# Optimization experiments

Measured on AMD Instinct MI355X. Metric: run time of the kernel, lower is better.

The kernel has to match this reference:

```python
import jax, jax.numpy as jnp
import numpy as np


def setup_inputs() -> dict:
    key = jax.random.key(0)
    k1, k2, k3, k4 = jax.random.split(key, 4)
    B, N, Fin, Fout, K = 8, 256, 64, 64, 3
    H = jax.random.normal(k1, (B, N, N, Fin), dtype=jnp.float32)
    # static Chebyshev polynomial stacks T_0..T_{K-1} for origin / dest Laplacians
    cheb_L1 = jax.random.normal(k2, (K, N, N), dtype=jnp.float32) * 0.1
    cheb_L2 = jax.random.normal(k3, (K, N, N), dtype=jnp.float32) * 0.1
    # xavier_uniform over last two dims (fan_in=Fin, fan_out=Fout)
    limit = float(np.sqrt(6.0 / (Fin + Fout)))
    weights = jax.random.uniform(k4, (K, K, Fin, Fout), dtype=jnp.float32,
                                 minval=-limit, maxval=limit)
    bias = jnp.zeros((Fout,), dtype=jnp.float32)
    return {"H": H, "cheb_L1": cheb_L1, "cheb_L2": cheb_L2,
            "weights": weights, "bias": bias}


def reference(H, cheb_L1, cheb_L2, weights, bias):
    # H' = relu( sum_{i,j} T_i(L1) @_1 H @_2 T_j(L2) @_3 W_ij + b )
    # Step 1: left graph shift for all i at once: (K,B,N,N,F)
    H_x1 = jnp.einsum('kuv,bvwf->kbuwf', cheb_L1, H)
    # Step 2+3 fused: right shift by T_j, project by W_ij, accumulate over i,j
    out = jnp.einsum('kbuwf,lwz,klfo->buzo', H_x1, cheb_L2, weights)
    return jax.nn.relu(out + bias)
```

## Files before the change

kernel.cpp:

```cpp
#include <hip/hip_runtime.h>

typedef __attribute__((ext_vector_type(8))) short s16x8;
typedef __attribute__((ext_vector_type(4))) float f32x4;

#define MFMA16 __builtin_amdgcn_mfma_f32_16x16x32_bf16
#define WAITVM(N) asm volatile("s_waitcnt vmcnt(" #N ")" ::: "memory")
#define SBAR() asm volatile("s_barrier" ::: "memory")
#define WAITLGKM0() asm volatile("s_waitcnt lgkmcnt(0)" ::: "memory")
#define SCHEDB() __builtin_amdgcn_sched_barrier(0)

__device__ __forceinline__ short f2bf(float x) {
  union { float f; unsigned u; } c; c.f = x;
  unsigned r = (c.u + 0x7fffu + ((c.u >> 16) & 1u)) >> 16;
  return (short)r;
}

__device__ __forceinline__ void gld16(const void* g, void* l) {
  __builtin_amdgcn_global_load_lds(
      (const __attribute__((address_space(1))) unsigned*)g,
      (__attribute__((address_space(3))) unsigned*)l, 16, 0, 0);
}


__global__ __launch_bounds__(256) void k_cvt_l1(const float* __restrict__ L1,
                                                short* __restrict__ L1b) {
  int i = blockIdx.x * 256 + threadIdx.x;
  L1b[i] = f2bf(L1[i]);
}

__global__ __launch_bounds__(256) void k_build_l2cat(const float* __restrict__ L2,
                                                     short* __restrict__ L2cat) {
  __shared__ float t[32][33];
  const int l = blockIdx.z, w0 = blockIdx.x * 32, z0 = blockIdx.y * 32;
  const int tx = threadIdx.x, ty = threadIdx.y;
  const float* src = L2 + (size_t)l * 65536;
  for (int i = ty; i < 32; i += 8) t[i][tx] = src[(size_t)(w0 + i) * 256 + z0 + tx];
  __syncthreads();
  for (int i = ty; i < 32; i += 8)
    L2cat[(size_t)(z0 + i) * 768 + l * 256 + w0 + tx] = f2bf(t[tx][i]);
}

__global__ __launch_bounds__(256) void k_build_wt(const float* __restrict__ W,
                                                  short* __restrict__ WT) {
  for (int idx = threadIdx.x + blockIdx.x * 256; idx < 192 * 192; idx += 256 * gridDim.x) {
    int lo = idx / 192, kf = idx % 192;
    int l = lo / 64, o = lo & 63, k = kf / 64, f = kf & 63;
    WT[idx] = f2bf(W[(((size_t)(k * 3 + l) * 64 + f) << 6) + o]);
  }
}

__global__ __launch_bounds__(256) void k_cvt_ht(const float* __restrict__ H,
                                                short* __restrict__ HbT, int b0) {
  __shared__ float t[32][33];
  const int bc = blockIdx.z;
  const int wf0 = blockIdx.x * 32, v0 = blockIdx.y * 32;
  const int tx = threadIdx.x, ty = threadIdx.y;
  const float* src = H + ((size_t)(b0 + bc) * 256 + v0) * 16384;
  for (int i = ty; i < 32; i += 8) t[i][tx] = src[(size_t)i * 16384 + wf0 + tx];
  __syncthreads();
  short* dst = HbT + ((size_t)bc * 16384 + wf0) * 256;
  for (int i = ty; i < 32; i += 8) dst[(size_t)i * 256 + v0 + tx] = f2bf(t[tx][i]);
}

__global__ __launch_bounds__(256, 4) void k_s1(const short* __restrict__ L1b,
                                               const short* __restrict__ HbT,
                                               short* __restrict__ A2) {
  __shared__ __align__(16) short At[2][128 * 32];
  __shared__ __align__(16) short Bt[2][128 * 32];
  const int t = threadIdx.x, lane = t & 63, wid = t >> 6;
  const int n0 = blockIdx.x * 128;
  const int kk = blockIdx.y >> 1;
  const int u0 = (blockIdx.y & 1) * 128;
  const int bc = blockIdx.z;
  const short* Ag = L1b + (size_t)kk * 65536;
  const short* Bg = HbT + (size_t)bc * 16384 * 256;
  const int wm = wid >> 1, wn = wid & 1;
  const int srow = lane >> 2;
  const int selem = ((lane & 3) ^ ((lane >> 3) & 3)) * 8;
  const int koff = ((lane >> 4) ^ ((lane >> 1) & 3)) * 8;
  const int ar = lane & 15;
#pragma unroll
  for (int j = 0; j < 2; ++j) {
    const int rb = wid * 32 + j * 16;
    gld16(Ag + (size_t)(u0 + rb + srow) * 256 + selem, At[0] + rb * 32);
    gld16(Bg + (size_t)(n0 + rb + srow) * 256 + selem, Bt[0] + rb * 32);
  }
  __syncthreads();
  f32x4 acc[4][4] = {};
#pragma unroll
  for (int kt8 = 0; kt8 < 8; ++kt8) {
    const int cur = kt8 & 1;
    s16x8 a[4], b[4];
#pragma unroll
    for (int i = 0; i < 4; ++i)
      a[i] = *(const s16x8*)&At[cur][(wm * 64 + i * 16 + ar) * 32 + koff];
#pragma unroll
    for (int j = 0; j < 4; ++j)
      b[j] = *(const s16x8*)&Bt[cur][(wn * 64 + j * 16 + ar) * 32 + koff];
    if (kt8 < 7) {
#pragma unroll
      for (int j = 0; j < 2; ++j) {
        const int rb = wid * 32 + j * 16;
        gld16(Ag + (size_t)(u0 + rb + srow) * 256 + (kt8 + 1) * 32 + selem, At[cur ^ 1] + rb * 32);
        gld16(Bg + (size_t)(n0 + rb + srow) * 256 + (kt8 + 1) * 32 + selem, Bt[cur ^ 1] + rb * 32);
      }
    }
#pragma unroll
    for (int i = 0; i < 4; ++i)
#pragma unroll
      for (int j = 0; j < 4; ++j) acc[i][j] = MFMA16(a[i], b[j], acc[i][j], 0, 0, 0);
    __syncthreads();
  }
  const int cr = lane >> 4, cc = lane & 15;
#pragma unroll
  for (int i = 0; i < 4; ++i)
#pragma unroll
    for (int j = 0; j < 4; ++j) {
      const int ncol = n0 + wn * 64 + j * 16 + cc;
      const int w = ncol >> 6, f = ncol & 63;
#pragma unroll
      for (int r = 0; r < 4; ++r) {
        const int u = u0 + wm * 64 + i * 16 + cr * 4 + r;
        A2[(((size_t)bc * 256 + u) * 256 + w) * 192 + kk * 64 + f] = f2bf(acc[i][j][r]);
      }
    }
}

__global__ __launch_bounds__(512, 4) void k_s23(const short* __restrict__ A2,
                                                const short* __restrict__ WTg,
                                                const short* __restrict__ L2cat,
                                                const float* __restrict__ bias,
                                                float* __restrict__ out, int b0) {
  __shared__ __align__(16) short P[64 * 256];
  __shared__ __align__(16) short AtS[8][3][32 * 32];
  short* Ws = P;
  const int t = threadIdx.x, lane = t & 63, wid = t >> 6;
  const int bul = blockIdx.x;
  const int ar = lane & 15, cc = ar, cr = lane >> 4, sl = lane & 7, ks = lane >> 4;
  const int srow = lane >> 2;
  const int selem = ((lane & 3) ^ ((lane >> 3) & 3)) * 8;
  const int koff = ((lane >> 4) ^ ((lane >> 1) & 3)) * 8;
  const short* A2g = A2 + (size_t)bul * 49152;

#define P1S(tt, bi)                                                                        \
  do {                                                                                     \
    gld16(A2g + (size_t)(wid * 32 + srow) * 192 + (tt) * 32 + selem, &AtS[wid][bi][0]);    \
    gld16(A2g + (size_t)(wid * 32 + 16 + srow) * 192 + (tt) * 32 + selem,                  \
          &AtS[wid][bi][512]);                                                             \
  } while (0)
#define P2S(tt, bi)                                                                        \
  do {                                                                                     \
    gld16(L2cat + (size_t)(wid * 32 + srow) * 768 + (tt) * 32 + selem, &AtS[wid][bi][0]);  \
    gld16(L2cat + (size_t)(wid * 32 + 16 + srow) * 768 + (tt) * 32 + selem,                \
          &AtS[wid][bi][512]);                                                             \
  } while (0)

  f32x4 acc2[2][4] = {};
#pragma unroll
  for (int l = 0; l < 3; ++l) {
    const short* WTl = WTg + (size_t)l * 64 * 192;
    for (int s = wid; s < 24; s += 8) {
      const int t6 = s / 4, g = (s & 3) * 16;
      gld16(WTl + (size_t)(g + srow) * 192 + t6 * 32 + selem, Ws + ((size_t)t6 * 64 + g) * 32);
    }
    P1S(0, 0);
    P1S(1, 1);
    P1S(2, 2);
    WAITVM(6);
    SBAR();

    f32x4 acc[4][2] = {};
#pragma unroll
    for (int kt6 = 0; kt6 < 6; ++kt6) {
      if (kt6 < 4) { WAITVM(4); } else if (kt6 == 4) { WAITVM(2); } else { WAITVM(0); }
      const short* stc = &AtS[wid][kt6 % 3][0];
      s16x8 a0 = *(const s16x8*)&stc[(0 + ar) * 32 + koff];
      s16x8 a1 = *(const s16x8*)&stc[(16 + ar) * 32 + koff];
#pragma unroll
      for (int j2 = 0; j2 < 4; ++j2) {
        s16x8 b = *(const s16x8*)&Ws[((size_t)kt6 * 64 + j2 * 16 + ar) * 32 + koff];
        acc[j2][0] = MFMA16(a0, b, acc[j2][0], 0, 0, 0);
        acc[j2][1] = MFMA16(a1, b, acc[j2][1], 0, 0, 0);
      }
      SCHEDB();
      if (kt6 == 0) { P1S(3, 0); } else if (kt6 == 1) { P1S(4, 1); } else if (kt6 == 2) { P1S(5, 2); }
    }
    WAITLGKM0();
    SBAR();

    P2S(l * 8 + 0, 0);
    P2S(l * 8 + 1, 1);
    P2S(l * 8 + 2, 2);

#pragma unroll
    for (int j2 = 0; j2 < 4; ++j2)
#pragma unroll
      for (int i = 0; i < 2; ++i)
#pragma unroll
        for (int rp = 0; rp < 2; ++rp) {
          const int r = rp * 2;
          const int w = wid * 32 + i * 16 + cr * 4 + r;
          const int o = j2 * 16 + cc;
          const int addr = o * 256 + (((w >> 3) ^ (o & 7)) << 3) + (w & 7);
          unsigned lo16 = (unsigned short)f2bf(acc[j2][i][r]);
          unsigned hi16 = (unsigned short)f2bf(acc[j2][i][r + 1]);
          *(unsigned*)&P[addr] = lo16 | (hi16 << 16);
        }
    WAITLGKM0();
    SBAR();

#pragma unroll
    for (int t2 = 0; t2 < 8; ++t2) {
      if (t2 < 6) { WAITVM(4); } else if (t2 == 6) { WAITVM(2); } else { WAITVM(0); }
      const short* stc = &AtS[wid][t2 % 3][0];
      s16x8 a0 = *(const s16x8*)&stc[(0 + ar) * 32 + koff];
      s16x8 a1 = *(const s16x8*)&stc[(16 + ar) * 32 + koff];
      const int S = t2 * 4 + ks;
#pragma unroll
      for (int j = 0; j < 4; ++j) {
        s16x8 b = *(const s16x8*)&P[(j * 16 + ar) * 256 + ((S ^ sl) << 3)];
        acc2[0][j] = MFMA16(a0, b, acc2[0][j], 0, 0, 0);
        acc2[1][j] = MFMA16(a1, b, acc2[1][j], 0, 0, 0);
      }
      SCHEDB();
      if (t2 < 5) {
        if (t2 % 3 == 0) { P2S(l * 8 + t2 + 3, 0); }
        else if (t2 % 3 == 1) { P2S(l * 8 + t2 + 3, 1); }
        else { P2S(l * 8 + t2 + 3, 2); }
      }
    }
    if (l < 2) {
      WAITLGKM0();
      SBAR();
    }
  }
#undef P1S
#undef P2S

  float* og = out + ((size_t)b0 * 256 + bul) * 16384;
#pragma unroll
  for (int i = 0; i < 2; ++i)
#pragma unroll
    for (int j = 0; j < 4; ++j) {
      const float bv = bias[j * 16 + cc];
#pragma unroll
      for (int r = 0; r < 4; ++r) {
        const int z = wid * 32 + i * 16 + cr * 4 + r;
        og[(size_t)z * 64 + j * 16 + cc] = fmaxf(acc2[i][j][r] + bv, 0.f);
      }
    }
}

extern "C" void kernel_launch(void* const* d_in, const int* in_sizes, int n_in,
                              void* d_out, int out_size, void* d_ws, size_t ws_size,
                              hipStream_t stream) {
  const float* H    = (const float*)d_in[0];
  const float* L1   = (const float*)d_in[1];
  const float* L2   = (const float*)d_in[2];
  const float* W    = (const float*)d_in[3];
  const float* bias = (const float*)d_in[4];
  float* out = (float*)d_out;

  char* ws = (char*)d_ws;
  short* L1b   = (short*)ws;
  short* L2cat = (short*)(ws + (384 << 10));
  short* WT    = (short*)(ws + (768 << 10));
  char* data = ws + (4ull << 20);

  const size_t perb = 32ull << 20;
  size_t avail = (ws_size > (4ull << 20)) ? ws_size - (4ull << 20) : 0;
  int nb = 1;
  if (avail >= 8 * perb) nb = 8;
  else if (avail >= 4 * perb) nb = 4;
  else if (avail >= 2 * perb) nb = 2;

  short* HbT = (short*)data;
  short* A2  = (short*)(data + (size_t)nb * (8ull << 20));

  k_cvt_l1<<<768, 256, 0, stream>>>(L1, L1b);
  k_build_l2cat<<<dim3(8, 8, 3), dim3(32, 8), 0, stream>>>(L2, L2cat);
  k_build_wt<<<36, 256, 0, stream>>>(W, WT);

  for (int b0 = 0; b0 < 8; b0 += nb) {
    k_cvt_ht<<<dim3(512, 8, nb), dim3(32, 8), 0, stream>>>(H, HbT, b0);
    k_s1<<<dim3(128, 6, nb), 256, 0, stream>>>(L1b, HbT, A2);
    k_s23<<<nb * 256, 512, 0, stream>>>(A2, WT, L2cat, bias, out, b0);
  }
}
```

Before: 322.1 us.

## Load L1 operand directly from global and transpose final MFMA for vectorized stores

```diff
diff --git a/kernel.cpp b/kernel.cpp
--- a/kernel.cpp
+++ b/kernel.cpp
@@ -65,7 +65,6 @@
 __global__ __launch_bounds__(256, 4) void k_s1(const short* __restrict__ L1b,
                                                const short* __restrict__ HbT,
                                                short* __restrict__ A2) {
-  __shared__ __align__(16) short At[2][128 * 32];
   __shared__ __align__(16) short Bt[2][128 * 32];
   const int t = threadIdx.x, lane = t & 63, wid = t >> 6;
   const int n0 = blockIdx.x * 128;
@@ -78,11 +77,10 @@
   const int srow = lane >> 2;
   const int selem = ((lane & 3) ^ ((lane >> 3) & 3)) * 8;
   const int koff = ((lane >> 4) ^ ((lane >> 1) & 3)) * 8;
-  const int ar = lane & 15;
+  const int ar = lane & 15, ks8 = (lane >> 4) * 8;
 #pragma unroll
   for (int j = 0; j < 2; ++j) {
     const int rb = wid * 32 + j * 16;
-    gld16(Ag + (size_t)(u0 + rb + srow) * 256 + selem, At[0] + rb * 32);
     gld16(Bg + (size_t)(n0 + rb + srow) * 256 + selem, Bt[0] + rb * 32);
   }
   __syncthreads();
@@ -93,7 +91,7 @@
     s16x8 a[4], b[4];
 #pragma unroll
     for (int i = 0; i < 4; ++i)
-      a[i] = *(const s16x8*)&At[cur][(wm * 64 + i * 16 + ar) * 32 + koff];
+      a[i] = *(const s16x8*)&Ag[(size_t)(u0 + wm * 64 + i * 16 + ar) * 256 + kt8 * 32 + ks8];
 #pragma unroll
     for (int j = 0; j < 4; ++j)
       b[j] = *(const s16x8*)&Bt[cur][(wn * 64 + j * 16 + ar) * 32 + koff];
@@ -101,7 +99,6 @@
 #pragma unroll
       for (int j = 0; j < 2; ++j) {
         const int rb = wid * 32 + j * 16;
-        gld16(Ag + (size_t)(u0 + rb + srow) * 256 + (kt8 + 1) * 32 + selem, At[cur ^ 1] + rb * 32);
         gld16(Bg + (size_t)(n0 + rb + srow) * 256 + (kt8 + 1) * 32 + selem, Bt[cur ^ 1] + rb * 32);
       }
     }
@@ -136,7 +133,7 @@
   short* Ws = P;
   const int t = threadIdx.x, lane = t & 63, wid = t >> 6;
   const int bul = blockIdx.x;
-  const int ar = lane & 15, cc = ar, cr = lane >> 4, sl = lane & 7, ks = lane >> 4;
+  const int ar = lane & 15, cc = ar, cr = lane >> 4, ks = lane >> 4;
   const int srow = lane >> 2;
   const int selem = ((lane & 3) ^ ((lane >> 3) & 3)) * 8;
   const int koff = ((lane >> 4) ^ ((lane >> 1) & 3)) * 8;
@@ -155,7 +152,7 @@
           &AtS[wid][bi][512]);                                                             \
   } while (0)
 
-  f32x4 acc2[2][4] = {};
+  f32x4 acc2[4][2] = {};
 #pragma unroll
   for (int l = 0; l < 3; ++l) {
     const short* WTl = WTg + (size_t)l * 64 * 192;
@@ -213,14 +210,14 @@
     for (int t2 = 0; t2 < 8; ++t2) {
       if (t2 < 6) { WAITVM(4); } else if (t2 == 6) { WAITVM(2); } else { WAITVM(0); }
       const short* stc = &AtS[wid][t2 % 3][0];
-      s16x8 a0 = *(const s16x8*)&stc[(0 + ar) * 32 + koff];
-      s16x8 a1 = *(const s16x8*)&stc[(16 + ar) * 32 + koff];
+      s16x8 bz0 = *(const s16x8*)&stc[(0 + ar) * 32 + koff];
+      s16x8 bz1 = *(const s16x8*)&stc[(16 + ar) * 32 + koff];
       const int S = t2 * 4 + ks;
 #pragma unroll
-      for (int j = 0; j < 4; ++j) {
-        s16x8 b = *(const s16x8*)&P[(j * 16 + ar) * 256 + ((S ^ sl) << 3)];
-        acc2[0][j] = MFMA16(a0, b, acc2[0][j], 0, 0, 0);
-        acc2[1][j] = MFMA16(a1, b, acc2[1][j], 0, 0, 0);
+      for (int m = 0; m < 4; ++m) {
+        s16x8 pa = *(const s16x8*)&P[(m * 16 + ar) * 256 + (((S ^ (ar & 7)) & 31) << 3)];
+        acc2[m][0] = MFMA16(pa, bz0, acc2[m][0], 0, 0, 0);
+        acc2[m][1] = MFMA16(pa, bz1, acc2[m][1], 0, 0, 0);
       }
       SCHEDB();
       if (t2 < 5) {
@@ -239,16 +236,20 @@
 
   float* og = out + ((size_t)b0 * 256 + bul) * 16384;
 #pragma unroll
-  for (int i = 0; i < 2; ++i)
-#pragma unroll
-    for (int j = 0; j < 4; ++j) {
-      const float bv = bias[j * 16 + cc];
-#pragma unroll
-      for (int r = 0; r < 4; ++r) {
-        const int z = wid * 32 + i * 16 + cr * 4 + r;
-        og[(size_t)z * 64 + j * 16 + cc] = fmaxf(acc2[i][j][r] + bv, 0.f);
-      }
-    }
+  for (int m = 0; m < 4; ++m) {
+    const int o = m * 16 + cr * 4;
+    const float4 bv = *(const float4*)&bias[o];
+#pragma unroll
+    for (int jz = 0; jz < 2; ++jz) {
+      const int z = wid * 32 + jz * 16 + cc;
+      float4 v;
+      v.x = fmaxf(acc2[m][jz][0] + bv.x, 0.f);
+      v.y = fmaxf(acc2[m][jz][1] + bv.y, 0.f);
+      v.z = fmaxf(acc2[m][jz][2] + bv.z, 0.f);
+      v.w = fmaxf(acc2[m][jz][3] + bv.w, 0.f);
+      *(float4*)&og[(size_t)z * 64 + o] = v;
+    }
+  }
 }
 
 extern "C" void kernel_launch(void* const* d_in, const int* in_sizes, int n_in,
```

Measured after the change: 347.4 us. +7.8%, slower.

## Enlarge s1 tile to full 256 rows with 512 threads; pack bf16 stores in transpose

Applied to the files above, without the earlier changes.

```diff
diff --git a/kernel.cpp b/kernel.cpp
--- a/kernel.cpp
+++ b/kernel.cpp
@@ -51,26 +51,29 @@
 
 __global__ __launch_bounds__(256) void k_cvt_ht(const float* __restrict__ H,
                                                 short* __restrict__ HbT, int b0) {
-  __shared__ float t[32][33];
+  __shared__ float t[64][33];
   const int bc = blockIdx.z;
-  const int wf0 = blockIdx.x * 32, v0 = blockIdx.y * 32;
+  const int wf0 = blockIdx.x * 32, v0 = blockIdx.y * 64;
   const int tx = threadIdx.x, ty = threadIdx.y;
   const float* src = H + ((size_t)(b0 + bc) * 256 + v0) * 16384;
-  for (int i = ty; i < 32; i += 8) t[i][tx] = src[(size_t)i * 16384 + wf0 + tx];
+  for (int i = ty; i < 64; i += 8) t[i][tx] = src[(size_t)i * 16384 + wf0 + tx];
   __syncthreads();
-  short* dst = HbT + ((size_t)bc * 16384 + wf0) * 256;
-  for (int i = ty; i < 32; i += 8) dst[(size_t)i * 256 + v0 + tx] = f2bf(t[tx][i]);
-}
-
-__global__ __launch_bounds__(256, 4) void k_s1(const short* __restrict__ L1b,
+  short* dst = HbT + ((size_t)bc * 16384 + wf0) * 256 + v0;
+  for (int i = ty; i < 32; i += 8) {
+    unsigned lo16 = (unsigned short)f2bf(t[tx * 2][i]);
+    unsigned hi16 = (unsigned short)f2bf(t[tx * 2 + 1][i]);
+    *(unsigned*)&dst[(size_t)i * 256 + tx * 2] = lo16 | (hi16 << 16);
+  }
+}
+
+__global__ __launch_bounds__(512, 3) void k_s1(const short* __restrict__ L1b,
                                                const short* __restrict__ HbT,
                                                short* __restrict__ A2) {
-  __shared__ __align__(16) short At[2][128 * 32];
+  __shared__ __align__(16) short At[2][256 * 32];
   __shared__ __align__(16) short Bt[2][128 * 32];
   const int t = threadIdx.x, lane = t & 63, wid = t >> 6;
   const int n0 = blockIdx.x * 128;
-  const int kk = blockIdx.y >> 1;
-  const int u0 = (blockIdx.y & 1) * 128;
+  const int kk = blockIdx.y;
   const int bc = blockIdx.z;
   const short* Ag = L1b + (size_t)kk * 65536;
   const short* Bg = HbT + (size_t)bc * 16384 * 256;
@@ -79,12 +82,14 @@
   const int selem = ((lane & 3) ^ ((lane >> 3) & 3)) * 8;
   const int koff = ((lane >> 4) ^ ((lane >> 1) & 3)) * 8;
   const int ar = lane & 15;
-#pragma unroll
-  for (int j = 0; j < 2; ++j) {
-    const int rb = wid * 32 + j * 16;
-    gld16(Ag + (size_t)(u0 + rb + srow) * 256 + selem, At[0] + rb * 32);
-    gld16(Bg + (size_t)(n0 + rb + srow) * 256 + selem, Bt[0] + rb * 32);
-  }
+#define S1STAGE(kt, bi)                                                                   \
+  do {                                                                                    \
+    const int ra0 = wid * 32, ra1 = wid * 32 + 16, rb = wid * 16;                         \
+    gld16(Ag + (size_t)(ra0 + srow) * 256 + (kt) * 32 + selem, At[bi] + ra0 * 32);        \
+    gld16(Ag + (size_t)(ra1 + srow) * 256 + (kt) * 32 + selem, At[bi] + ra1 * 32);        \
+    gld16(Bg + (size_t)(n0 + rb + srow) * 256 + (kt) * 32 + selem, Bt[bi] + rb * 32);     \
+  } while (0)
+  S1STAGE(0, 0);
   __syncthreads();
   f32x4 acc[4][4] = {};
 #pragma unroll
@@ -97,20 +102,14 @@
 #pragma unroll
     for (int j = 0; j < 4; ++j)
       b[j] = *(const s16x8*)&Bt[cur][(wn * 64 + j * 16 + ar) * 32 + koff];
-    if (kt8 < 7) {
-#pragma unroll
-      for (int j = 0; j < 2; ++j) {
-        const int rb = wid * 32 + j * 16;
-        gld16(Ag + (size_t)(u0 + rb + srow) * 256 + (kt8 + 1) * 32 + selem, At[cur ^ 1] + rb * 32);
-        gld16(Bg + (size_t)(n0 + rb + srow) * 256 + (kt8 + 1) * 32 + selem, Bt[cur ^ 1] + rb * 32);
-      }
-    }
+    if (kt8 < 7) { S1STAGE(kt8 + 1, cur ^ 1); }
 #pragma unroll
     for (int i = 0; i < 4; ++i)
 #pragma unroll
       for (int j = 0; j < 4; ++j) acc[i][j] = MFMA16(a[i], b[j], acc[i][j], 0, 0, 0);
     __syncthreads();
   }
+#undef S1STAGE
   const int cr = lane >> 4, cc = lane & 15;
 #pragma unroll
   for (int i = 0; i < 4; ++i)
@@ -120,7 +119,7 @@
       const int w = ncol >> 6, f = ncol & 63;
 #pragma unroll
       for (int r = 0; r < 4; ++r) {
-        const int u = u0 + wm * 64 + i * 16 + cr * 4 + r;
+        const int u = wm * 64 + i * 16 + cr * 4 + r;
         A2[(((size_t)bc * 256 + u) * 256 + w) * 192 + kk * 64 + f] = f2bf(acc[i][j][r]);
       }
     }
@@ -282,8 +281,8 @@
   k_build_wt<<<36, 256, 0, stream>>>(W, WT);
 
   for (int b0 = 0; b0 < 8; b0 += nb) {
-    k_cvt_ht<<<dim3(512, 8, nb), dim3(32, 8), 0, stream>>>(H, HbT, b0);
-    k_s1<<<dim3(128, 6, nb), 256, 0, stream>>>(L1b, HbT, A2);
+    k_cvt_ht<<<dim3(512, 4, nb), dim3(32, 8), 0, stream>>>(H, HbT, b0);
+    k_s1<<<dim3(128, 3, nb), 512, 0, stream>>>(L1b, HbT, A2);
     k_s23<<<nb * 256, 512, 0, stream>>>(A2, WT, L2cat, bias, out, b0);
   }
 }
```

Result: faster. 288.7 us, median of 2 (-10.4%).
